# Kernel tuning notes

Hardware: AMD Instinct MI355X
Metric: run time of the kernel (lower is better)

The kernel has to match this reference:

```python
import jax, jax.numpy as jnp
import numpy as np

SHIFT = 1  # module's random shift_direction, fixed to +1 for determinism
B, C, H, W_SP = 1024, 512, 7, 7


def setup_inputs() -> dict:
    key = jax.random.key(0)
    k1, k2 = jax.random.split(key)
    x = jax.random.normal(k1, (B, C, H, W_SP), dtype=jnp.float32)
    W = jax.random.normal(k2, (256, 3, 3, 512), dtype=jnp.float32)
    return {"x": x, "W": W}


def _forward(x, W):
    # unfold along H with kernel (3,1), padding (1,0):
    # patches[b,c,kh,h,w] = x_padded[b,c,h+kh,w]
    xp = jnp.pad(x, ((0, 0), (0, 0), (1, 1), (0, 0)))
    t2 = jnp.stack([xp[:, :, k:k + H, :] for k in range(3)], axis=2)  # (B,512,3,7,7)
    # split channels 512 -> (2,256), move group dim next to H
    t2 = t2.reshape(B, 2, 256, 3, H, W_SP)
    t2 = t2.transpose(0, 2, 3, 4, 1, 5)          # (B,256,3,7,2,7)
    t2 = t2.reshape(B, 256, 3, 14, W_SP)         # interleave (h,group) -> 14
    t2 = jnp.roll(t2, SHIFT, axis=3)             # shift along interleaved dim
    t2 = t2.reshape(B, 256, 3, 7, 2, W_SP).sum(axis=4)  # (B,256,3,7,7)
    t2 = t2.transpose(0, 1, 3, 2, 4)             # (B,256,7,3,7) = (m,l,n,j,w)
    # second shift + unfold along w with kernel 3, padding 1
    t3 = jnp.roll(t2, SHIFT, axis=4)
    tp = jnp.pad(t3, ((0, 0), (0, 0), (0, 0), (0, 0), (1, 1)))
    t3u = jnp.stack([tp[..., k:k + W_SP] for k in range(3)], axis=4)  # (B,256,7,3,3,7) = (m,l,n,j,k,p)
    # torch einsum 'mlnjok, ljki -> mnoi' with o = output position, k = kernel tap
    out = jnp.einsum('mlnjkp,ljki->mpni', t3u, W)  # wait: check axis order below
    # Note: torch permutes (m,c,h,j,kernel,pos)->(m,c,h,j,pos,kernel) before einsum,
    # so contraction is over (l,j,kernel) and output is (m, n=h, o=pos, i).
    out = jnp.einsum('mlnjkp,ljki->mnpi', t3u, W)  # (B,7,7,512)
    return out.transpose(0, 3, 1, 2)              # (B,512,7,7)


def reference(x, W):
    return _forward(x, W)
```

## Files before the change

### kernel.cpp

```cpp
#include <hip/hip_runtime.h>
#include <hip/hip_bf16.h>


typedef __bf16 bf16x8 __attribute__((ext_vector_type(8)));
typedef float f32x4 __attribute__((ext_vector_type(4)));

#define VT_OFFSET (4u << 20)
#define VT_BYTES  (7168ull * 7 * 768 * 2)
#define WS_NEED   (VT_OFFSET + VT_BYTES)

__global__ __launch_bounds__(256) void prep_w(const float* __restrict__ Wg,
                                              __bf16* __restrict__ W2) {
    int idx = blockIdx.x * 256 + threadIdx.x;
    int i = idx / 2304;
    int kk = idx - i * 2304;
    int tap = kk / 768;
    int c = kk - tap * 768;
    W2[idx] = (__bf16)Wg[(c * 3 + tap) * 512 + i];
}

__global__ __launch_bounds__(256) void prep_v(const float* __restrict__ x,
                                              __bf16* __restrict__ Vt) {
    __shared__ float xs[256 * 49];
    const int b = blockIdx.x >> 1;
    const int g = blockIdx.x & 1;
    const int tid = threadIdx.x;

    {
        const float4* src0 = (const float4*)(x + ((size_t)b * 512 + g * 128) * 49);
        const float4* src1 = (const float4*)(x + ((size_t)b * 512 + 256 + g * 128) * 49);
        float4* dst0 = (float4*)xs;
        float4* dst1 = (float4*)(xs + 128 * 49);
        #pragma unroll
        for (int it = 0; it < 7; ++it) {
            const int q = it * 256 + tid;
            if (q < 1568) dst0[q] = src0[q];
        }
        #pragma unroll
        for (int it = 0; it < 7; ++it) {
            const int q = it * 256 + tid;
            if (q < 1568) dst1[q] = src1[q];
        }
    }
    __syncthreads();

    for (int h = 0; h < 7; ++h) {
        const int hm = (h + 6) % 7;
        for (int it = 0; it < 2; ++it) {
            const int u = it * 256 + tid;
            if (u < 336) {
                const int r = u / 48;
                const int k = u - r * 48;
                const int w = (r + 6) % 7;
                bf16x8 vv;
                #pragma unroll
                for (int e = 0; e < 8; ++e) {
                    const int c = k * 8 + e;
                    const int l = c / 3;
                    const int j = c - 3 * l;
                    const int r1 = h + j - 1;
                    const int r2 = hm + j - 1;
                    float v = 0.f;
                    if (r1 >= 0 && r1 < 7) v += xs[l * 49 + r1 * 7 + w];
                    if (r2 >= 0 && r2 < 7) v += xs[(128 + l) * 49 + r2 * 7 + w];
                    vv[e] = (__bf16)v;
                }
                *(bf16x8*)(Vt + (size_t)((b * 7 + h) * 7 + r) * 768 + g * 384 + k * 8) = vv;
            }
        }
    }
}

__global__ __launch_bounds__(256) void gemm_vt(const __bf16* __restrict__ Vt,
                                               const __bf16* __restrict__ W2,
                                               float* __restrict__ out) {
    __shared__ __bf16 T[16 * 400];
    __shared__ __bf16 Bt[128 * 104];

    const int tid = threadIdx.x;
    const int g0 = blockIdx.x;
    const int nb = (g0 >> 3) & 3;
    const int mb = ((g0 >> 5) << 3) | (g0 & 7);
    const int i0 = nb * 128;

    for (int q = tid; q < 3200; q += 256) ((int*)T)[q] = 0;

    const int lane = tid & 63;
    const int wave = tid >> 6;
    const int wm = wave >> 1;
    const int wn = wave & 1;
    const int ln15 = lane & 15;
    const int gq = lane >> 4;

    f32x4 acc[4][4];
    #pragma unroll
    for (int a = 0; a < 4; ++a)
        #pragma unroll
        for (int bq = 0; bq < 4; ++bq) acc[a][bq] = (f32x4){0.f, 0.f, 0.f, 0.f};

    __syncthreads();

    for (int chunk = 0; chunk < 24; ++chunk) {
        #pragma unroll
        for (int it = 0; it < 2; ++it) {
            const int u = it * 256 + tid;
            if (u < 448) {
                const int q = u & 3;
                const int tmp = u >> 2;
                const int t = tmp % 7;
                const int bh = tmp / 7;
                const float4 val = *(const float4*)(
                    Vt + (size_t)((mb * 16 + bh) * 7 + t) * 768 + chunk * 32 + q * 8);
                *(float4*)(&T[bh * 400 + (t + 1) * 40 + q * 8]) = val;
            }
        }
        #pragma unroll
        for (int it = 0; it < 6; ++it) {
            const int u = it * 256 + tid;
            const int tap = u >> 9;
            const int rem = u & 511;
            const int n = rem >> 2;
            const int q = rem & 3;
            const float4 val = *(const float4*)(W2 + (size_t)(i0 + n) * 2304 +
                                                tap * 768 + chunk * 32 + q * 8);
            *(float4*)(&Bt[n * 104 + tap * 32 + q * 8]) = val;
        }

        __syncthreads();

        #pragma unroll
        for (int tap = 0; tap < 3; ++tap) {
            bf16x8 af[4], bfr[4];
            #pragma unroll
            for (int mf = 0; mf < 4; ++mf) {
                const int bh_l = wm * 8 + mf * 2 + (ln15 >> 3);
                const int p = ln15 & 7;
                af[mf] = *(const bf16x8*)(&T[(bh_l * 10 + p + tap) * 40 + gq * 8]);
            }
            #pragma unroll
            for (int nf = 0; nf < 4; ++nf) {
                const int n_l = wn * 64 + nf * 16 + ln15;
                bfr[nf] = *(const bf16x8*)(&Bt[n_l * 104 + tap * 32 + gq * 8]);
            }
            #pragma unroll
            for (int mf = 0; mf < 4; ++mf)
                #pragma unroll
                for (int nf = 0; nf < 4; ++nf)
                    acc[mf][nf] = __builtin_amdgcn_mfma_f32_16x16x32_bf16(
                        af[mf], bfr[nf], acc[mf][nf], 0, 0, 0);
        }

        __syncthreads();
    }

    #pragma unroll
    for (int mf = 0; mf < 4; ++mf) {
        #pragma unroll
        for (int r = 0; r < 4; ++r) {
            const int mrow = gq * 4 + r;
            const int Mg_l = wm * 64 + mf * 16 + mrow;
            const int p = Mg_l & 7;
            if (p == 7) continue;
            const int bh_l = Mg_l >> 3;
            const int bhg = mb * 16 + bh_l;
            const int b = bhg / 7;
            const int h = bhg - 7 * b;
            #pragma unroll
            for (int nf = 0; nf < 4; ++nf) {
                const int i = i0 + wn * 64 + nf * 16 + ln15;
                out[(((size_t)b * 512 + i) * 7 + h) * 7 + p] = acc[mf][nf][r];
            }
        }
    }
}

__global__ __launch_bounds__(256) void gemm_shift(const float* __restrict__ x,
                                                  const __bf16* __restrict__ W2,
                                                  float* __restrict__ out) {
    __shared__ __bf16 T[16 * 10 * 40];
    __shared__ __bf16 Bt[128 * 104];

    const int tid = threadIdx.x;
    const int mb = blockIdx.x >> 2;
    const int nb = blockIdx.x & 3;
    const int i0 = nb * 128;

    const int cl  = tid & 31;
    const int bh0 = tid >> 5;
    const int bhg0 = mb * 16 + bh0;
    const int bhg1 = bhg0 + 8;
    const int b0 = bhg0 / 7, h0 = bhg0 - 7 * b0;
    const int b1 = bhg1 / 7, h1 = bhg1 - 7 * b1;
    const int hm0 = (h0 + 6) % 7, hm1 = (h1 + 6) % 7;

    for (int q = tid; q < 16 * 10 * 40 / 2; q += 256) ((int*)T)[q] = 0;

    const int lane = tid & 63;
    const int wave = tid >> 6;
    const int wm = wave >> 1;
    const int wn = wave & 1;
    const int ln15 = lane & 15;
    const int gq = lane >> 4;

    f32x4 acc[4][4];
    #pragma unroll
    for (int a = 0; a < 4; ++a)
        #pragma unroll
        for (int bq = 0; bq < 4; ++bq) acc[a][bq] = (f32x4){0.f, 0.f, 0.f, 0.f};

    __syncthreads();

    for (int chunk = 0; chunk < 24; ++chunk) {
        const int cg = chunk * 32 + cl;
        const int l = cg / 3;
        const int j = cg - 3 * l;
        {
            const int r1 = h0 + j - 1, r2 = hm0 + j - 1;
            float v[7] = {0.f, 0.f, 0.f, 0.f, 0.f, 0.f, 0.f};
            if (r1 >= 0 && r1 < 7) {
                const float* p1 = x + (((size_t)b0 * 512 + l) * 7 + r1) * 7;
                #pragma unroll
                for (int w = 0; w < 7; ++w) v[w] += p1[w];
            }
            if (r2 >= 0 && r2 < 7) {
                const float* p2 = x + (((size_t)b0 * 512 + 256 + l) * 7 + r2) * 7;
                #pragma unroll
                for (int w = 0; w < 7; ++w) v[w] += p2[w];
            }
            #pragma unroll
            for (int w = 0; w < 7; ++w)
                T[bh0 * 400 + ((w + 1) % 7 + 1) * 40 + cl] = (__bf16)v[w];
        }
        {
            const int r1 = h1 + j - 1, r2 = hm1 + j - 1;
            float v[7] = {0.f, 0.f, 0.f, 0.f, 0.f, 0.f, 0.f};
            if (r1 >= 0 && r1 < 7) {
                const float* p1 = x + (((size_t)b1 * 512 + l) * 7 + r1) * 7;
                #pragma unroll
                for (int w = 0; w < 7; ++w) v[w] += p1[w];
            }
            if (r2 >= 0 && r2 < 7) {
                const float* p2 = x + (((size_t)b1 * 512 + 256 + l) * 7 + r2) * 7;
                #pragma unroll
                for (int w = 0; w < 7; ++w) v[w] += p2[w];
            }
            #pragma unroll
            for (int w = 0; w < 7; ++w)
                T[(bh0 + 8) * 400 + ((w + 1) % 7 + 1) * 40 + cl] = (__bf16)v[w];
        }

        #pragma unroll
        for (int it = 0; it < 6; ++it) {
            const int u = it * 256 + tid;
            const int tap = u >> 9;
            const int rem = u & 511;
            const int n = rem >> 2;
            const int q = rem & 3;
            const float4 val = *(const float4*)(W2 + (size_t)(i0 + n) * 2304 +
                                                tap * 768 + chunk * 32 + q * 8);
            *(float4*)(&Bt[n * 104 + tap * 32 + q * 8]) = val;
        }

        __syncthreads();

        #pragma unroll
        for (int tap = 0; tap < 3; ++tap) {
            bf16x8 af[4], bfr[4];
            #pragma unroll
            for (int mf = 0; mf < 4; ++mf) {
                const int bh_l = wm * 8 + mf * 2 + (ln15 >> 3);
                const int p = ln15 & 7;
                af[mf] = *(const bf16x8*)(&T[(bh_l * 10 + p + tap) * 40 + gq * 8]);
            }
            #pragma unroll
            for (int nf = 0; nf < 4; ++nf) {
                const int n_l = wn * 64 + nf * 16 + ln15;
                bfr[nf] = *(const bf16x8*)(&Bt[n_l * 104 + tap * 32 + gq * 8]);
            }
            #pragma unroll
            for (int mf = 0; mf < 4; ++mf)
                #pragma unroll
                for (int nf = 0; nf < 4; ++nf)
                    acc[mf][nf] = __builtin_amdgcn_mfma_f32_16x16x32_bf16(
                        af[mf], bfr[nf], acc[mf][nf], 0, 0, 0);
        }

        __syncthreads();
    }

    #pragma unroll
    for (int mf = 0; mf < 4; ++mf) {
        #pragma unroll
        for (int r = 0; r < 4; ++r) {
            const int mrow = gq * 4 + r;
            const int Mg_l = wm * 64 + mf * 16 + mrow;
            const int p = Mg_l & 7;
            if (p == 7) continue;
            const int bh_l = Mg_l >> 3;
            const int bhg = mb * 16 + bh_l;
            const int b = bhg / 7;
            const int h = bhg - 7 * b;
            #pragma unroll
            for (int nf = 0; nf < 4; ++nf) {
                const int i = i0 + wn * 64 + nf * 16 + ln15;
                out[(((size_t)b * 512 + i) * 7 + h) * 7 + p] = acc[mf][nf][r];
            }
        }
    }
}

extern "C" void kernel_launch(void* const* d_in, const int* in_sizes, int n_in,
                              void* d_out, int out_size, void* d_ws, size_t ws_size,
                              hipStream_t stream) {
    const float* x  = (const float*)d_in[0];
    const float* Wg = (const float*)d_in[1];
    float* out = (float*)d_out;
    __bf16* W2 = (__bf16*)d_ws;

    prep_w<<<dim3(512 * 2304 / 256), dim3(256), 0, stream>>>(Wg, W2);

    if (ws_size >= WS_NEED) {
        __bf16* Vt = (__bf16*)((char*)d_ws + VT_OFFSET);
        prep_v<<<dim3(2048), dim3(256), 0, stream>>>(x, Vt);
        gemm_vt<<<dim3(448 * 4), dim3(256), 0, stream>>>(Vt, W2, out);
    } else {
        gemm_shift<<<dim3(448 * 4), dim3(256), 0, stream>>>(x, W2, out);
    }
}
```

Baseline: 393.5 us.

## Double-buffer weight tiles via direct global-to-LDS loads and dense M tiling in gemm_vt

gemm_vt now streams the weight tile into a double-buffered LDS array with global_load_lds, prefetching the next chunk while computing the current one. The activation tile is no longer staged in LDS. Each lane reads its A fragments straight from global Vt with tap offsets, masking the row-boundary taps to zero. The M tiling becomes dense (128 real rows per block, no padded 8th position), so the grid shrinks from 448 to 392 row blocks. The intent is to cut LDS staging, padding waste and load latency, at the cost of uncoalesced global A reads that rely on cache reuse.

Measured after the change: 517.2 us. 1.31x slower.

```diff
diff --git a/kernel.cpp b/kernel.cpp
--- a/kernel.cpp
+++ b/kernel.cpp
@@ -4,10 +4,17 @@
 
 typedef __bf16 bf16x8 __attribute__((ext_vector_type(8)));
 typedef float f32x4 __attribute__((ext_vector_type(4)));
+typedef unsigned int u32;
 
 #define VT_OFFSET (4u << 20)
 #define VT_BYTES  (7168ull * 7 * 768 * 2)
 #define WS_NEED   (VT_OFFSET + VT_BYTES)
+
+__device__ __forceinline__ void gload_lds16(const void* g, void* l) {
+    __builtin_amdgcn_global_load_lds(
+        (const __attribute__((address_space(1))) u32*)g,
+        (__attribute__((address_space(3))) u32*)l, 16, 0, 0);
+}
 
 __global__ __launch_bounds__(256) void prep_w(const float* __restrict__ Wg,
                                               __bf16* __restrict__ W2) {
@@ -74,16 +81,13 @@
 __global__ __launch_bounds__(256) void gemm_vt(const __bf16* __restrict__ Vt,
                                                const __bf16* __restrict__ W2,
                                                float* __restrict__ out) {
-    __shared__ __bf16 T[16 * 400];
-    __shared__ __bf16 Bt[128 * 104];
+    __shared__ __bf16 Bt[2][12288];
 
     const int tid = threadIdx.x;
     const int g0 = blockIdx.x;
     const int nb = (g0 >> 3) & 3;
     const int mb = ((g0 >> 5) << 3) | (g0 & 7);
     const int i0 = nb * 128;
-
-    for (int q = tid; q < 3200; q += 256) ((int*)T)[q] = 0;
 
     const int lane = tid & 63;
     const int wave = tid >> 6;
@@ -92,28 +96,176 @@
     const int ln15 = lane & 15;
     const int gq = lane >> 4;
 
+    int soff[6];
+    #pragma unroll
+    for (int it = 0; it < 6; ++it) {
+        const int u = it * 256 + tid;
+        const int tap = u >> 9;
+        const int rem = u & 511;
+        const int n = rem >> 2;
+        const int q = rem & 3;
+        soff[it] = ((i0 + n) * 2304 + tap * 768 + q * 8) * 2;
+    }
+
+    int aoff[4], md7[4];
+    #pragma unroll
+    for (int mf = 0; mf < 4; ++mf) {
+        const int m = mb * 128 + wm * 64 + mf * 16 + ln15;
+        aoff[mf] = m * 1536 + gq * 16;
+        md7[mf] = m % 7;
+    }
+
+    bf16x8 zero8;
+    #pragma unroll
+    for (int e = 0; e < 8; ++e) zero8[e] = (__bf16)0.f;
+
     f32x4 acc[4][4];
     #pragma unroll
     for (int a = 0; a < 4; ++a)
         #pragma unroll
         for (int bq = 0; bq < 4; ++bq) acc[a][bq] = (f32x4){0.f, 0.f, 0.f, 0.f};
 
+    const char* VtB = (const char*)Vt;
+    const char* W2B = (const char*)W2;
+
+    #pragma unroll
+    for (int it = 0; it < 6; ++it)
+        gload_lds16(W2B + soff[it], &Bt[0][it * 2048 + tid * 8]);
     __syncthreads();
 
     for (int chunk = 0; chunk < 24; ++chunk) {
-        #pragma unroll
-        for (int it = 0; it < 2; ++it) {
-            const int u = it * 256 + tid;
-            if (u < 448) {
-                const int q = u & 3;
-                const int tmp = u >> 2;
-                const int t = tmp % 7;
-                const int bh = tmp / 7;
-                const float4 val = *(const float4*)(
-                    Vt + (size_t)((mb * 16 + bh) * 7 + t) * 768 + chunk * 32 + q * 8);
-                *(float4*)(&T[bh * 400 + (t + 1) * 40 + q * 8]) = val;
-            }
-        }
+        const int cur = chunk & 1;
+        if (chunk < 23) {
+            const int ck2 = (chunk + 1) * 64;
+            #pragma unroll
+            for (int it = 0; it < 6; ++it)
+                gload_lds16(W2B + soff[it] + ck2,
+                            &Bt[cur ^ 1][it * 2048 + tid * 8]);
+        }
+        const int ck = chunk * 64;
+
+        #pragma unroll
+        for (int tap = 0; tap < 3; ++tap) {
+            bf16x8 af[4], bfr[4];
+            #pragma unroll
+            for (int mf = 0; mf < 4; ++mf) {
+                af[mf] = zero8;
+                bool ok;
+                if (tap == 0)      ok = (md7[mf] != 0);
+                else if (tap == 2) ok = (md7[mf] != 6);
+                else               ok = true;
+                if (ok)
+                    af[mf] = *(const bf16x8*)(VtB + aoff[mf] + (tap - 1) * 1536 + ck);
+            }
+            #pragma unroll
+            for (int nf = 0; nf < 4; ++nf) {
+                const int n_l = wn * 64 + nf * 16 + ln15;
+                bfr[nf] = *(const bf16x8*)(&Bt[cur][tap * 4096 + n_l * 32 + gq * 8]);
+            }
+            #pragma unroll
+            for (int mf = 0; mf < 4; ++mf)
+                #pragma unroll
+                for (int nf = 0; nf < 4; ++nf)
+                    acc[mf][nf] = __builtin_amdgcn_mfma_f32_16x16x32_bf16(
+                        af[mf], bfr[nf], acc[mf][nf], 0, 0, 0);
+        }
+
+        __syncthreads();
+    }
+
+    #pragma unroll
+    for (int mf = 0; mf < 4; ++mf) {
+        #pragma unroll
+        for (int r = 0; r < 4; ++r) {
+            const int m = mb * 128 + wm * 64 + mf * 16 + gq * 4 + r;
+            const int bh = m / 7;
+            const int p = m - 7 * bh;
+            const int b = bh / 7;
+            const int h = bh - 7 * b;
+            #pragma unroll
+            for (int nf = 0; nf < 4; ++nf) {
+                const int i = i0 + wn * 64 + nf * 16 + ln15;
+                out[(((size_t)b * 512 + i) * 7 + h) * 7 + p] = acc[mf][nf][r];
+            }
+        }
+    }
+}
+
+__global__ __launch_bounds__(256) void gemm_shift(const float* __restrict__ x,
+                                                  const __bf16* __restrict__ W2,
+                                                  float* __restrict__ out) {
+    __shared__ __bf16 T[16 * 10 * 40];
+    __shared__ __bf16 Bt[128 * 104];
+
+    const int tid = threadIdx.x;
+    const int mb = blockIdx.x >> 2;
+    const int nb = blockIdx.x & 3;
+    const int i0 = nb * 128;
+
+    const int cl  = tid & 31;
+    const int bh0 = tid >> 5;
+    const int bhg0 = mb * 16 + bh0;
+    const int bhg1 = bhg0 + 8;
+    const int b0 = bhg0 / 7, h0 = bhg0 - 7 * b0;
+    const int b1 = bhg1 / 7, h1 = bhg1 - 7 * b1;
+    const int hm0 = (h0 + 6) % 7, hm1 = (h1 + 6) % 7;
+
+    for (int q = tid; q < 16 * 10 * 40 / 2; q += 256) ((int*)T)[q] = 0;
+
+    const int lane = tid & 63;
+    const int wave = tid >> 6;
+    const int wm = wave >> 1;
+    const int wn = wave & 1;
+    const int ln15 = lane & 15;
+    const int gq = lane >> 4;
+
+    f32x4 acc[4][4];
+    #pragma unroll
+    for (int a = 0; a < 4; ++a)
+        #pragma unroll
+        for (int bq = 0; bq < 4; ++bq) acc[a][bq] = (f32x4){0.f, 0.f, 0.f, 0.f};
+
+    __syncthreads();
+
+    for (int chunk = 0; chunk < 24; ++chunk) {
+        const int cg = chunk * 32 + cl;
+        const int l = cg / 3;
+        const int j = cg - 3 * l;
+        {
+            const int r1 = h0 + j - 1, r2 = hm0 + j - 1;
+            float v[7] = {0.f, 0.f, 0.f, 0.f, 0.f, 0.f, 0.f};
+            if (r1 >= 0 && r1 < 7) {
+                const float* p1 = x + (((size_t)b0 * 512 + l) * 7 + r1) * 7;
+                #pragma unroll
+                for (int w = 0; w < 7; ++w) v[w] += p1[w];
+            }
+            if (r2 >= 0 && r2 < 7) {
+                const float* p2 = x + (((size_t)b0 * 512 + 256 + l) * 7 + r2) * 7;
+                #pragma unroll
+                for (int w = 0; w < 7; ++w) v[w] += p2[w];
+            }
+            #pragma unroll
+            for (int w = 0; w < 7; ++w)
+                T[bh0 * 400 + ((w + 1) % 7 + 1) * 40 + cl] = (__bf16)v[w];
+        }
+        {
+            const int r1 = h1 + j - 1, r2 = hm1 + j - 1;
+            float v[7] = {0.f, 0.f, 0.f, 0.f, 0.f, 0.f, 0.f};
+            if (r1 >= 0 && r1 < 7) {
+                const float* p1 = x + (((size_t)b1 * 512 + l) * 7 + r1) * 7;
+                #pragma unroll
+                for (int w = 0; w < 7; ++w) v[w] += p1[w];
+            }
+            if (r2 >= 0 && r2 < 7) {
+                const float* p2 = x + (((size_t)b1 * 512 + 256 + l) * 7 + r2) * 7;
+                #pragma unroll
+                for (int w = 0; w < 7; ++w) v[w] += p2[w];
+            }
+            #pragma unroll
+            for (int w = 0; w < 7; ++w)
+                T[(bh0 + 8) * 400 + ((w + 1) % 7 + 1) * 40 + cl] = (__bf16)v[w];
+        }
+
         #pragma unroll
         for (int it = 0; it < 6; ++it) {
             const int u = it * 256 + tid;
@@ -174,141 +326,6 @@
     }
 }
 
-__global__ __launch_bounds__(256) void gemm_shift(const float* __restrict__ x,
-                                                  const __bf16* __restrict__ W2,
-                                                  float* __restrict__ out) {
-    __shared__ __bf16 T[16 * 10 * 40];
-    __shared__ __bf16 Bt[128 * 104];
-
-    const int tid = threadIdx.x;
-    const int mb = blockIdx.x >> 2;
-    const int nb = blockIdx.x & 3;
-    const int i0 = nb * 128;
-
-    const int cl  = tid & 31;
-    const int bh0 = tid >> 5;
-    const int bhg0 = mb * 16 + bh0;
-    const int bhg1 = bhg0 + 8;
-    const int b0 = bhg0 / 7, h0 = bhg0 - 7 * b0;
-    const int b1 = bhg1 / 7, h1 = bhg1 - 7 * b1;
-    const int hm0 = (h0 + 6) % 7, hm1 = (h1 + 6) % 7;
-
-    for (int q = tid; q < 16 * 10 * 40 / 2; q += 256) ((int*)T)[q] = 0;
-
-    const int lane = tid & 63;
-    const int wave = tid >> 6;
-    const int wm = wave >> 1;
-    const int wn = wave & 1;
-    const int ln15 = lane & 15;
-    const int gq = lane >> 4;
-
-    f32x4 acc[4][4];
-    #pragma unroll
-    for (int a = 0; a < 4; ++a)
-        #pragma unroll
-        for (int bq = 0; bq < 4; ++bq) acc[a][bq] = (f32x4){0.f, 0.f, 0.f, 0.f};
-
-    __syncthreads();
-
-    for (int chunk = 0; chunk < 24; ++chunk) {
-        const int cg = chunk * 32 + cl;
-        const int l = cg / 3;
-        const int j = cg - 3 * l;
-        {
-            const int r1 = h0 + j - 1, r2 = hm0 + j - 1;
-            float v[7] = {0.f, 0.f, 0.f, 0.f, 0.f, 0.f, 0.f};
-            if (r1 >= 0 && r1 < 7) {
-                const float* p1 = x + (((size_t)b0 * 512 + l) * 7 + r1) * 7;
-                #pragma unroll
-                for (int w = 0; w < 7; ++w) v[w] += p1[w];
-            }
-            if (r2 >= 0 && r2 < 7) {
-                const float* p2 = x + (((size_t)b0 * 512 + 256 + l) * 7 + r2) * 7;
-                #pragma unroll
-                for (int w = 0; w < 7; ++w) v[w] += p2[w];
-            }
-            #pragma unroll
-            for (int w = 0; w < 7; ++w)
-                T[bh0 * 400 + ((w + 1) % 7 + 1) * 40 + cl] = (__bf16)v[w];
-        }
-        {
-            const int r1 = h1 + j - 1, r2 = hm1 + j - 1;
-            float v[7] = {0.f, 0.f, 0.f, 0.f, 0.f, 0.f, 0.f};
-            if (r1 >= 0 && r1 < 7) {
-                const float* p1 = x + (((size_t)b1 * 512 + l) * 7 + r1) * 7;
-                #pragma unroll
-                for (int w = 0; w < 7; ++w) v[w] += p1[w];
-            }
-            if (r2 >= 0 && r2 < 7) {
-                const float* p2 = x + (((size_t)b1 * 512 + 256 + l) * 7 + r2) * 7;
-                #pragma unroll
-                for (int w = 0; w < 7; ++w) v[w] += p2[w];
-            }
-            #pragma unroll
-            for (int w = 0; w < 7; ++w)
-                T[(bh0 + 8) * 400 + ((w + 1) % 7 + 1) * 40 + cl] = (__bf16)v[w];
-        }
-
-        #pragma unroll
-        for (int it = 0; it < 6; ++it) {
-            const int u = it * 256 + tid;
-            const int tap = u >> 9;
-            const int rem = u & 511;
-            const int n = rem >> 2;
-            const int q = rem & 3;
-            const float4 val = *(const float4*)(W2 + (size_t)(i0 + n) * 2304 +
-                                                tap * 768 + chunk * 32 + q * 8);
-            *(float4*)(&Bt[n * 104 + tap * 32 + q * 8]) = val;
-        }
-
-        __syncthreads();
-
-        #pragma unroll
-        for (int tap = 0; tap < 3; ++tap) {
-            bf16x8 af[4], bfr[4];
-            #pragma unroll
-            for (int mf = 0; mf < 4; ++mf) {
-                const int bh_l = wm * 8 + mf * 2 + (ln15 >> 3);
-                const int p = ln15 & 7;
-                af[mf] = *(const bf16x8*)(&T[(bh_l * 10 + p + tap) * 40 + gq * 8]);
-            }
-            #pragma unroll
-            for (int nf = 0; nf < 4; ++nf) {
-                const int n_l = wn * 64 + nf * 16 + ln15;
-                bfr[nf] = *(const bf16x8*)(&Bt[n_l * 104 + tap * 32 + gq * 8]);
-            }
-            #pragma unroll
-            for (int mf = 0; mf < 4; ++mf)
-                #pragma unroll
-                for (int nf = 0; nf < 4; ++nf)
-                    acc[mf][nf] = __builtin_amdgcn_mfma_f32_16x16x32_bf16(
-                        af[mf], bfr[nf], acc[mf][nf], 0, 0, 0);
-        }
-
-        __syncthreads();
-    }
-
-    #pragma unroll
-    for (int mf = 0; mf < 4; ++mf) {
-        #pragma unroll
-        for (int r = 0; r < 4; ++r) {
-            const int mrow = gq * 4 + r;
-            const int Mg_l = wm * 64 + mf * 16 + mrow;
-            const int p = Mg_l & 7;
-            if (p == 7) continue;
-            const int bh_l = Mg_l >> 3;
-            const int bhg = mb * 16 + bh_l;
-            const int b = bhg / 7;
-            const int h = bhg - 7 * b;
-            #pragma unroll
-            for (int nf = 0; nf < 4; ++nf) {
-                const int i = i0 + wn * 64 + nf * 16 + ln15;
-                out[(((size_t)b * 512 + i) * 7 + h) * 7 + p] = acc[mf][nf][r];
-            }
-        }
-    }
-}
-
 extern "C" void kernel_launch(void* const* d_in, const int* in_sizes, int n_in,
                               void* d_out, int out_size, void* d_ws, size_t ws_size,
                               hipStream_t stream) {
@@ -322,7 +339,7 @@
     if (ws_size >= WS_NEED) {
         __bf16* Vt = (__bf16*)((char*)d_ws + VT_OFFSET);
         prep_v<<<dim3(2048), dim3(256), 0, stream>>>(x, Vt);
-        gemm_vt<<<dim3(448 * 4), dim3(256), 0, stream>>>(Vt, W2, out);
+        gemm_vt<<<dim3(392 * 4), dim3(256), 0, stream>>>(Vt, W2, out);
     } else {
         gemm_shift<<<dim3(448 * 4), dim3(256), 0, stream>>>(x, W2, out);
     }
```
